# Performance work log

Hardware: AMD Instinct MI355X
Metric: run time of the kernel (lower is better)

The kernel has to match this reference:

```python
import jax, jax.numpy as jnp
import numpy as np

B, S, D_IN, D_OUT = 8, 2048, 1024, 1024

def setup_inputs() -> dict:
    key = jax.random.key(0)
    ks = jax.random.split(key, 6)
    return {
        "inputs_for_keys": jax.random.normal(ks[0], (B, S, D_IN), dtype=jnp.float32),
        "inputs_for_values": jax.random.normal(ks[1], (B, S, D_IN), dtype=jnp.float32),
        "inputs_for_queries": jax.random.normal(ks[2], (B, S, D_IN), dtype=jnp.float32),
        "W_K": jax.random.normal(ks[3], (D_IN, D_OUT), dtype=jnp.float32) * 0.05,
        "W_V": jax.random.normal(ks[4], (D_IN, D_OUT), dtype=jnp.float32) * 0.05,
        "W_Q": jax.random.normal(ks[5], (D_IN, D_OUT), dtype=jnp.float32) * 0.05,
    }

def reference(inputs_for_keys, inputs_for_values, inputs_for_queries, W_K, W_V, W_Q):
    # Linear projections: [B,S,D_in] @ [D_in,D_out] -> [B,S,D_out]
    K = jnp.einsum("bsd,de->bse", inputs_for_keys, W_K)
    V = jnp.einsum("bsd,de->bse", inputs_for_values, W_V)
    Q = jnp.einsum("bsd,de->bse", inputs_for_queries, W_Q)
    scale = jnp.sqrt(jnp.asarray(K.shape[-1], dtype=K.dtype))
    # Scaled dot-product attention scores: [B,Sq,Sk]
    scores = jnp.einsum("bqe,bke->bqk", Q, K) / scale
    probs = jax.nn.softmax(scores, axis=-1)
    Z = jnp.einsum("bqk,bke->bqe", probs, V)
    return Z
```

## Files before the change

### kernel.cpp

```cpp
#include <hip/hip_runtime.h>
#include <hip/hip_bf16.h>
#include <stdint.h>

#define BATCH 8
#define SEQ 2048
#define DMODEL 1024

typedef __attribute__((ext_vector_type(4))) float f32x4;
typedef __attribute__((ext_vector_type(8))) short bf16x8;
typedef __attribute__((ext_vector_type(4))) uint32_t u32x4;
typedef __attribute__((ext_vector_type(2))) uint32_t u32x2;

#define MFMA16(a, b, c) __builtin_amdgcn_mfma_f32_16x16x32_bf16((a), (b), (c), 0, 0, 0)


static __device__ __forceinline__ uint16_t f2bf(float f) {
    uint32_t u = __builtin_bit_cast(uint32_t, f);
    u += 0x7fffu + ((u >> 16) & 1u);
    return (uint16_t)(u >> 16);
}
static __device__ __forceinline__ uint32_t pk2(float lo, float hi) {
    return (uint32_t)f2bf(lo) | ((uint32_t)f2bf(hi) << 16);
}
static __device__ __forceinline__ void gload16(const uint16_t* g, uint16_t* l) {
    __builtin_amdgcn_global_load_lds((const __attribute__((address_space(1))) void*)g,
                                     (__attribute__((address_space(3))) void*)l, 16, 0, 0);
}

__global__ __launch_bounds__(256) void cast_bf16_pk(const float* __restrict__ src,
                                                    uint16_t* __restrict__ dst) {
    const size_t c = (size_t)blockIdx.x * 256 + threadIdx.x;
    const size_t panel = c >> 11;
    const int w = (int)(c & 2047);
    const int ks = w >> 4, r15 = w & 15;
    const float* s = src + (panel * 16 + r15) * DMODEL + ks * 8;
    f32x4 a = *(const f32x4*)s;
    f32x4 b = *(const f32x4*)(s + 4);
    u32x4 o = {pk2(a[0], a[1]), pk2(a[2], a[3]), pk2(b[0], b[1]), pk2(b[2], b[3])};
    *(u32x4*)(dst + c * 8) = o;
}

__global__ void wt_cast_kernel(const float* __restrict__ Wk, const float* __restrict__ Wv,
                               const float* __restrict__ Wq, uint16_t* __restrict__ WT) {
    const float* W = blockIdx.z == 0 ? Wk : (blockIdx.z == 1 ? Wv : Wq);
    uint16_t* dst = WT + (size_t)blockIdx.z * DMODEL * DMODEL;
    __shared__ float tile[32][33];
    const int x = blockIdx.x * 32, y = blockIdx.y * 32;
    const int tx = threadIdx.x, ty = threadIdx.y;
#pragma unroll
    for (int j = 0; j < 4; j++)
        tile[ty * 4 + j][tx] = W[(size_t)(y + ty * 4 + j) * DMODEL + x + tx];
    __syncthreads();
#pragma unroll
    for (int j = 0; j < 4; j++) {
        const int n = x + ty * 4 + j, k = y + tx;
        const size_t off = ((size_t)(n >> 4) * (DMODEL / 8) + (k >> 3)) * 128 +
                           (n & 15) * 8 + (k & 7);
        dst[off] = f2bf(tile[tx][ty * 4 + j]);
    }
}

#define STG_A(kt, sl, h)                                                          \
    do {                                                                          \
        const size_t g0 = (size_t)((h) * 8 + (tid >> 7)) * eldA +                 \
                          (size_t)(kt) * 1024 + (tid & 127) * 8;                  \
        gload16(Ab + g0, &As[sl][(h) * 8192 + tid * 8]);                          \
        gload16(Ab + g0 + 4 * eldA, &As[sl][(h) * 8192 + tid * 8 + 4096]);        \
    } while (0)
#define STG_B(kt, sl, h)                                                          \
    do {                                                                          \
        const size_t g0 = (size_t)((h) * 8 + (tid >> 7)) * eldB +                 \
                          (size_t)(kt) * 1024 + (tid & 127) * 8;                  \
        gload16(Bb + g0, &Bs[sl][(h) * 8192 + tid * 8]);                          \
        gload16(Bb + g0 + 4 * eldB, &Bs[sl][(h) * 8192 + tid * 8 + 4096]);        \
    } while (0)

#define READ_B(sl)                                                                \
    _Pragma("unroll") for (int j = 0; j < 4; j++) {                               \
        bfr[j][0] = *(const bf16x8*)&Bs[sl][(wc * 4 + j) * 1024 + lbase];         \
        bfr[j][1] = *(const bf16x8*)&Bs[sl][(wc * 4 + j) * 1024 + 512 + lbase];   \
    }

#define VM4 asm volatile("s_waitcnt vmcnt(4)" ::: "memory")
#define VM0 asm volatile("s_waitcnt vmcnt(0)" ::: "memory")
#define NOPW (void)0
#define NOST (void)0

#define PH(sl, q, STG, WAIT)                                                      \
    do {                                                                          \
        const int ab = (wr * 8 + 2 * (q)) * 1024 + lbase;                         \
        bf16x8 a00 = *(const bf16x8*)&As[sl][ab];                                 \
        bf16x8 a01 = *(const bf16x8*)&As[sl][ab + 512];                           \
        bf16x8 a10 = *(const bf16x8*)&As[sl][ab + 1024];                          \
        bf16x8 a11 = *(const bf16x8*)&As[sl][ab + 1536];                          \
        STG;                                                                      \
        WAIT;                                                                     \
        __builtin_amdgcn_s_barrier();                                             \
        asm volatile("s_waitcnt lgkmcnt(0)" ::: "memory");                        \
        __builtin_amdgcn_sched_barrier(0);                                        \
        __builtin_amdgcn_s_setprio(1);                                            \
        _Pragma("unroll") for (int j = 0; j < 4; j++) {                           \
            acc[2 * (q)][j] = MFMA16(a00, bfr[j][0], acc[2 * (q)][j]);            \
            acc[2 * (q)][j] = MFMA16(a01, bfr[j][1], acc[2 * (q)][j]);            \
            acc[2 * (q) + 1][j] = MFMA16(a10, bfr[j][0], acc[2 * (q) + 1][j]);    \
            acc[2 * (q) + 1][j] = MFMA16(a11, bfr[j][1], acc[2 * (q) + 1][j]);    \
        }                                                                         \
        __builtin_amdgcn_s_setprio(0);                                            \
        __builtin_amdgcn_s_barrier();                                             \
    } while (0)

template <int MODE, int BX>
__global__ __launch_bounds__(512, 2) void gemm8p(const uint16_t* __restrict__ Ag,
                                                 const uint16_t* __restrict__ Bg,
                                                 void* __restrict__ Cg,
                                                 const float* __restrict__ Linv,
                                                 float scale, int lda, int ldb, int ldc,
                                                 int nk, size_t sA, size_t sB, size_t sC) {
    __shared__ __align__(16) uint16_t As[2][16384];
    __shared__ __align__(16) uint16_t Bs[2][16384];
    const int bz = BX ? blockIdx.x : blockIdx.z;
    const int bm = BX ? blockIdx.y : blockIdx.x;
    const int bn = BX ? blockIdx.z : blockIdx.y;
    const int m0 = bm * 256, n0 = bn * 256;
    const uint16_t* Ab = Ag + (size_t)bz * sA + (size_t)m0 * lda;
    const uint16_t* Bb = Bg + (size_t)bz * sB + (size_t)n0 * ldb;
    const int tid = threadIdx.x, lane = tid & 63;
    const int wid = tid >> 6, wr = wid >> 2, wc = wid & 3;
    const int lr = lane & 15, lg = lane >> 4;
    const int lbase = lg * 128 + lr * 8;
    const size_t eldA = (size_t)lda * 16, eldB = (size_t)ldb * 16;

    f32x4 acc[8][4] = {};
    bf16x8 bfr[4][2];
    STG_A(0, 0, 0); STG_A(0, 0, 1);
    STG_B(0, 0, 0); STG_B(0, 0, 1);
    STG_B(1, 1, 0); STG_B(1, 1, 1);
    VM4;
    __builtin_amdgcn_s_barrier();
    for (int kt = 0; kt + 3 < nk; kt += 2) {
        READ_B(0);
        PH(0, 0, STG_A(kt + 1, 1, 0), NOPW);
        PH(0, 1, STG_A(kt + 1, 1, 1), NOPW);
        PH(0, 2, STG_B(kt + 2, 0, 0), NOPW);
        PH(0, 3, STG_B(kt + 2, 0, 1), VM4);
        READ_B(1);
        PH(1, 0, STG_A(kt + 2, 0, 0), NOPW);
        PH(1, 1, STG_A(kt + 2, 0, 1), NOPW);
        PH(1, 2, STG_B(kt + 3, 1, 0), NOPW);
        PH(1, 3, STG_B(kt + 3, 1, 1), VM4);
    }
    READ_B(0);
    PH(0, 0, STG_A(nk - 1, 1, 0), NOPW);
    PH(0, 1, STG_A(nk - 1, 1, 1), NOPW);
    PH(0, 2, NOST, NOPW);
    PH(0, 3, NOST, VM0);
    READ_B(1);
    PH(1, 0, NOST, NOPW);
    PH(1, 1, NOST, NOPW);
    PH(1, 2, NOST, NOPW);
    PH(1, 3, NOST, NOPW);

    if constexpr (MODE == 0) {
        uint16_t* C = (uint16_t*)Cg + (size_t)bz * sC;
#pragma unroll
        for (int i = 0; i < 8; i++) {
            const int gm = m0 + wr * 128 + i * 16 + lg * 4;
            const size_t pbase = (size_t)(gm >> 4) * (ldc / 8);
#pragma unroll
            for (int j = 0; j < 4; j++) {
                const int gn = n0 + wc * 64 + j * 16 + lr;
                const size_t off = (pbase + (gn >> 3)) * 128 + (gn & 7);
#pragma unroll
                for (int r = 0; r < 4; r++)
                    C[off + (lg * 4 + r) * 8] = f2bf(acc[i][j][r] * scale);
            }
        }
    } else if constexpr (MODE == 1) {
        uint16_t* C = (uint16_t*)Cg;
#pragma unroll
        for (int i = 0; i < 8; i++) {
            const int gm = m0 + wr * 128 + i * 16 + lg * 4;
            const int bb = gm / SEQ;
            const int s0 = gm - bb * SEQ;
            uint16_t* Cb = C + (size_t)bb * DMODEL * SEQ;
#pragma unroll
            for (int j = 0; j < 4; j++) {
                const int e = n0 + wc * 64 + j * 16 + lr;
                const size_t off = ((size_t)(e >> 4) * (SEQ / 8) + (s0 >> 3)) * 128 +
                                   (e & 15) * 8 + (s0 & 7);
                u32x2 v = {pk2(acc[i][j][0], acc[i][j][1]), pk2(acc[i][j][2], acc[i][j][3])};
                *(u32x2*)&Cb[off] = v;
            }
        }
    } else {
        float* C = (float*)Cg + (size_t)bz * sC;
        const float* LB = Linv + bz * SEQ;
#pragma unroll
        for (int i = 0; i < 8; i++) {
            const int gm = m0 + wr * 128 + i * 16 + lg * 4;
            const f32x4 lv = *(const f32x4*)&LB[gm];
#pragma unroll
            for (int j = 0; j < 4; j++) {
                const int gn = n0 + wc * 64 + j * 16 + lr;
#pragma unroll
                for (int r = 0; r < 4; r++)
                    C[(size_t)(gm + r) * ldc + gn] = acc[i][j][r] * lv[r];
            }
        }
    }
}

__global__ __launch_bounds__(256) void softmax_pk(uint16_t* __restrict__ S,
                                                  float* __restrict__ Linv) {
    const size_t panel = blockIdx.x;
    uint16_t* sp = S + panel * (size_t)(16 * SEQ);
    const int t = threadIdx.x, lane = t & 63, w = t >> 6;
    const int r15 = t & 15, ksl = t >> 4;
    __shared__ float rm[4][16], rs[4][16];
    u32x4 raw[16];
    float mx = -3.0e38f;
#pragma unroll
    for (int u = 0; u < 16; u++) {
        raw[u] = *(const u32x4*)&sp[(ksl + u * 16) * 128 + r15 * 8];
#pragma unroll
        for (int j = 0; j < 4; j++) {
            mx = fmaxf(mx, __builtin_bit_cast(float, raw[u][j] << 16));
            mx = fmaxf(mx, __builtin_bit_cast(float, raw[u][j] & 0xffff0000u));
        }
    }
    mx = fmaxf(mx, __shfl_xor(mx, 16));
    mx = fmaxf(mx, __shfl_xor(mx, 32));
    if (lane < 16) rm[w][lane] = mx;
    __syncthreads();
    const float m = fmaxf(fmaxf(rm[0][r15], rm[1][r15]), fmaxf(rm[2][r15], rm[3][r15]));
    float sum = 0.0f;
#pragma unroll
    for (int u = 0; u < 16; u++) {
#pragma unroll
        for (int j = 0; j < 4; j++) {
            float lo = __expf(__builtin_bit_cast(float, raw[u][j] << 16) - m);
            float hi = __expf(__builtin_bit_cast(float, raw[u][j] & 0xffff0000u) - m);
            sum += lo + hi;
            raw[u][j] = pk2(lo, hi);
        }
    }
    sum += __shfl_xor(sum, 16);
    sum += __shfl_xor(sum, 32);
    if (lane < 16) rs[w][lane] = sum;
    __syncthreads();
    const float tot = rs[0][r15] + rs[1][r15] + rs[2][r15] + rs[3][r15];
#pragma unroll
    for (int u = 0; u < 16; u++)
        *(u32x4*)&sp[(ksl + u * 16) * 128 + r15 * 8] = raw[u];
    if (w == 0 && lane < 16) Linv[panel * 16 + lane] = 1.0f / tot;
}

extern "C" void kernel_launch(void* const* d_in, const int* in_sizes, int n_in,
                              void* d_out, int out_size, void* d_ws, size_t ws_size,
                              hipStream_t stream) {
    const float* Xk = (const float*)d_in[0];
    const float* Xv = (const float*)d_in[1];
    const float* Xq = (const float*)d_in[2];
    const float* Wk = (const float*)d_in[3];
    const float* Wv = (const float*)d_in[4];
    const float* Wq = (const float*)d_in[5];
    float* out = (float*)d_out;
    char* ws = (char*)d_ws;
    uint16_t* Qbf = (uint16_t*)(ws);
    uint16_t* Kbf = (uint16_t*)(ws + (size_t)33554432);
    uint16_t* VTb = (uint16_t*)(ws + (size_t)67108864);
    uint16_t* WT  = (uint16_t*)(ws + (size_t)100663296);
    float*    Linv= (float*)(ws + (size_t)106954752);
    uint16_t* Sb  = (uint16_t*)(ws + (size_t)107020288);
    uint16_t* Xbf = (uint16_t*)(ws + (size_t)171966464);

    wt_cast_kernel<<<dim3(32, 32, 3), dim3(32, 8), 0, stream>>>(Wk, Wv, Wq, WT);
    cast_bf16_pk<<<8192, 256, 0, stream>>>(Xq, Xbf);
    gemm8p<0, 0><<<dim3(64, 4, 1), 512, 0, stream>>>(
        Xbf, WT + 2 * 1048576, (void*)Qbf, nullptr, 0.03125f,
        DMODEL, DMODEL, DMODEL, DMODEL / 64, 0, 0, 0);
    cast_bf16_pk<<<8192, 256, 0, stream>>>(Xk, Xbf);
    gemm8p<0, 0><<<dim3(64, 4, 1), 512, 0, stream>>>(
        Xbf, WT, (void*)Kbf, nullptr, 1.0f,
        DMODEL, DMODEL, DMODEL, DMODEL / 64, 0, 0, 0);
    cast_bf16_pk<<<8192, 256, 0, stream>>>(Xv, Xbf);
    gemm8p<1, 0><<<dim3(64, 4, 1), 512, 0, stream>>>(
        Xbf, WT + 1048576, (void*)VTb, nullptr, 1.0f,
        DMODEL, DMODEL, 0, DMODEL / 64, 0, 0, 0);
    gemm8p<0, 1><<<dim3(8, 8, 8), 512, 0, stream>>>(
        Qbf, Kbf, (void*)Sb, nullptr, 1.0f,
        DMODEL, DMODEL, SEQ, DMODEL / 64,
        (size_t)SEQ * DMODEL, (size_t)SEQ * DMODEL, (size_t)SEQ * SEQ);
    softmax_pk<<<dim3(BATCH * SEQ / 16), 256, 0, stream>>>(Sb, Linv);
    gemm8p<2, 1><<<dim3(8, 8, 4), 512, 0, stream>>>(
        Sb, VTb, (void*)out, Linv, 1.0f,
        SEQ, SEQ, DMODEL, SEQ / 64,
        (size_t)SEQ * SEQ, (size_t)DMODEL * SEQ, (size_t)SEQ * DMODEL);
}
```

Baseline: 369.7 us.

## Shrink GEMM tiles to 128x128 with 4-wave blocks for more parallelism

Replaces the 256x256-tile, 8-wave GEMM with a 128x128-tile, 4-wave variant that keeps the same double-buffered, phase-interleaved load/MFMA pipeline. The stage loads and per-phase fragments are rearranged for the smaller tiles, and all GEMM launches get four times as many blocks. The aim is better CU occupancy and load balance, since the old grids (256 or 512 blocks) poorly filled the GPU. The cost is lower data reuse per block, so more global and L2 traffic per FLOP, plus more barriers relative to compute.

```diff
diff --git a/kernel.cpp b/kernel.cpp
--- a/kernel.cpp
+++ b/kernel.cpp
@@ -60,111 +60,120 @@
     }
 }
 
-#define STG_A(kt, sl, h)                                                          \
-    do {                                                                          \
-        const size_t g0 = (size_t)((h) * 8 + (tid >> 7)) * eldA +                 \
-                          (size_t)(kt) * 1024 + (tid & 127) * 8;                  \
-        gload16(Ab + g0, &As[sl][(h) * 8192 + tid * 8]);                          \
-        gload16(Ab + g0 + 4 * eldA, &As[sl][(h) * 8192 + tid * 8 + 4096]);        \
+#define STG_A(kt, sl)                                                         \
+    do {                                                                      \
+        const size_t k0_ = (size_t)(kt) * 1024;                               \
+        gload16(Ab + k0_ + sbA,            &As[sl][tid * 8]);                 \
+        gload16(Ab + k0_ + sbA + 2 * eldA, &As[sl][tid * 8 + 2048]);          \
+        gload16(Ab + k0_ + sbA + 4 * eldA, &As[sl][tid * 8 + 4096]);          \
+        gload16(Ab + k0_ + sbA + 6 * eldA, &As[sl][tid * 8 + 6144]);          \
     } while (0)
-#define STG_B(kt, sl, h)                                                          \
-    do {                                                                          \
-        const size_t g0 = (size_t)((h) * 8 + (tid >> 7)) * eldB +                 \
-                          (size_t)(kt) * 1024 + (tid & 127) * 8;                  \
-        gload16(Bb + g0, &Bs[sl][(h) * 8192 + tid * 8]);                          \
-        gload16(Bb + g0 + 4 * eldB, &Bs[sl][(h) * 8192 + tid * 8 + 4096]);        \
+#define STG_B(kt, sl)                                                         \
+    do {                                                                      \
+        const size_t k0_ = (size_t)(kt) * 1024;                               \
+        gload16(Bb + k0_ + sbB,            &Bs[sl][tid * 8]);                 \
+        gload16(Bb + k0_ + sbB + 2 * eldB, &Bs[sl][tid * 8 + 2048]);          \
+        gload16(Bb + k0_ + sbB + 4 * eldB, &Bs[sl][tid * 8 + 4096]);          \
+        gload16(Bb + k0_ + sbB + 6 * eldB, &Bs[sl][tid * 8 + 6144]);          \
     } while (0)
 
-#define READ_B(sl)                                                                \
-    _Pragma("unroll") for (int j = 0; j < 4; j++) {                               \
-        bfr[j][0] = *(const bf16x8*)&Bs[sl][(wc * 4 + j) * 1024 + lbase];         \
-        bfr[j][1] = *(const bf16x8*)&Bs[sl][(wc * 4 + j) * 1024 + 512 + lbase];   \
-    }
-
-#define VM4 asm volatile("s_waitcnt vmcnt(4)" ::: "memory")
-#define VM0 asm volatile("s_waitcnt vmcnt(0)" ::: "memory")
-#define NOPW (void)0
+#define READ_B(sl)                                                            \
+    _Pragma("unroll") for (int j = 0; j < 4; j++) {                           \
+        bfr[j][0] = *(const bf16x8*)&Bs[sl][(wc * 4 + j) * 1024 + lbase];     \
+        bfr[j][1] = *(const bf16x8*)&Bs[sl][(wc * 4 + j) * 1024 + 512 + lbase]; \
+    }
+
+#define VMW4 asm volatile("s_waitcnt vmcnt(4)" ::: "memory")
+#define VMW0 asm volatile("s_waitcnt vmcnt(0)" ::: "memory")
+#define NOW (void)0
 #define NOST (void)0
 
-#define PH(sl, q, STG, WAIT)                                                      \
-    do {                                                                          \
-        const int ab = (wr * 8 + 2 * (q)) * 1024 + lbase;                         \
-        bf16x8 a00 = *(const bf16x8*)&As[sl][ab];                                 \
-        bf16x8 a01 = *(const bf16x8*)&As[sl][ab + 512];                           \
-        bf16x8 a10 = *(const bf16x8*)&As[sl][ab + 1024];                          \
-        bf16x8 a11 = *(const bf16x8*)&As[sl][ab + 1536];                          \
-        STG;                                                                      \
-        WAIT;                                                                     \
-        __builtin_amdgcn_s_barrier();                                             \
-        asm volatile("s_waitcnt lgkmcnt(0)" ::: "memory");                        \
-        __builtin_amdgcn_sched_barrier(0);                                        \
-        __builtin_amdgcn_s_setprio(1);                                            \
-        _Pragma("unroll") for (int j = 0; j < 4; j++) {                           \
-            acc[2 * (q)][j] = MFMA16(a00, bfr[j][0], acc[2 * (q)][j]);            \
-            acc[2 * (q)][j] = MFMA16(a01, bfr[j][1], acc[2 * (q)][j]);            \
-            acc[2 * (q) + 1][j] = MFMA16(a10, bfr[j][0], acc[2 * (q) + 1][j]);    \
-            acc[2 * (q) + 1][j] = MFMA16(a11, bfr[j][1], acc[2 * (q) + 1][j]);    \
-        }                                                                         \
-        __builtin_amdgcn_s_setprio(0);                                            \
-        __builtin_amdgcn_s_barrier();                                             \
+#define PH_CORE(r0, r1)                                                       \
+    __builtin_amdgcn_s_barrier();                                             \
+    asm volatile("s_waitcnt lgkmcnt(0)" ::: "memory");                        \
+    __builtin_amdgcn_sched_barrier(0);                                        \
+    __builtin_amdgcn_s_setprio(1);                                            \
+    _Pragma("unroll") for (int j = 0; j < 4; j++) {                           \
+        acc[r0][j] = MFMA16(a00, bfr[j][0], acc[r0][j]);                      \
+        acc[r0][j] = MFMA16(a01, bfr[j][1], acc[r0][j]);                      \
+        acc[r1][j] = MFMA16(a10, bfr[j][0], acc[r1][j]);                      \
+        acc[r1][j] = MFMA16(a11, bfr[j][1], acc[r1][j]);                      \
+    }                                                                         \
+    __builtin_amdgcn_s_setprio(0);                                            \
+    __builtin_amdgcn_s_barrier();
+
+#define PH0(sl, STG, WAIT)                                                    \
+    do {                                                                      \
+        READ_B(sl);                                                           \
+        const int ab_ = (wr * 4) * 1024 + lbase;                              \
+        bf16x8 a00 = *(const bf16x8*)&As[sl][ab_];                            \
+        bf16x8 a01 = *(const bf16x8*)&As[sl][ab_ + 512];                      \
+        bf16x8 a10 = *(const bf16x8*)&As[sl][ab_ + 1024];                     \
+        bf16x8 a11 = *(const bf16x8*)&As[sl][ab_ + 1536];                     \
+        STG;                                                                  \
+        WAIT;                                                                 \
+        PH_CORE(0, 1)                                                         \
     } while (0)
 
+#define PH1(sl, STG, WAIT)                                                    \
+    do {                                                                      \
+        const int ab_ = (wr * 4 + 2) * 1024 + lbase;                          \
+        bf16x8 a00 = *(const bf16x8*)&As[sl][ab_];                            \
+        bf16x8 a01 = *(const bf16x8*)&As[sl][ab_ + 512];                      \
+        bf16x8 a10 = *(const bf16x8*)&As[sl][ab_ + 1024];                     \
+        bf16x8 a11 = *(const bf16x8*)&As[sl][ab_ + 1536];                     \
+        STG;                                                                  \
+        WAIT;                                                                 \
+        PH_CORE(2, 3)                                                         \
+    } while (0)
+
 template <int MODE, int BX>
-__global__ __launch_bounds__(512, 2) void gemm8p(const uint16_t* __restrict__ Ag,
-                                                 const uint16_t* __restrict__ Bg,
-                                                 void* __restrict__ Cg,
-                                                 const float* __restrict__ Linv,
-                                                 float scale, int lda, int ldb, int ldc,
-                                                 int nk, size_t sA, size_t sB, size_t sC) {
-    __shared__ __align__(16) uint16_t As[2][16384];
-    __shared__ __align__(16) uint16_t Bs[2][16384];
+__global__ __launch_bounds__(256, 2) void gemm128(const uint16_t* __restrict__ Ag,
+                                                  const uint16_t* __restrict__ Bg,
+                                                  void* __restrict__ Cg,
+                                                  const float* __restrict__ Linv,
+                                                  float scale, int lda, int ldb, int ldc,
+                                                  int nk, size_t sA, size_t sB, size_t sC) {
+    __shared__ __align__(16) uint16_t As[2][8192];
+    __shared__ __align__(16) uint16_t Bs[2][8192];
     const int bz = BX ? blockIdx.x : blockIdx.z;
     const int bm = BX ? blockIdx.y : blockIdx.x;
     const int bn = BX ? blockIdx.z : blockIdx.y;
-    const int m0 = bm * 256, n0 = bn * 256;
+    const int m0 = bm * 128, n0 = bn * 128;
     const uint16_t* Ab = Ag + (size_t)bz * sA + (size_t)m0 * lda;
     const uint16_t* Bb = Bg + (size_t)bz * sB + (size_t)n0 * ldb;
     const int tid = threadIdx.x, lane = tid & 63;
-    const int wid = tid >> 6, wr = wid >> 2, wc = wid & 3;
+    const int wid = tid >> 6, wr = wid >> 1, wc = wid & 1;
     const int lr = lane & 15, lg = lane >> 4;
     const int lbase = lg * 128 + lr * 8;
     const size_t eldA = (size_t)lda * 16, eldB = (size_t)ldb * 16;
-
-    f32x4 acc[8][4] = {};
+    const size_t sbA = (size_t)(tid >> 7) * eldA + (tid & 127) * 8;
+    const size_t sbB = (size_t)(tid >> 7) * eldB + (tid & 127) * 8;
+
+    f32x4 acc[4][4] = {};
     bf16x8 bfr[4][2];
-    STG_A(0, 0, 0); STG_A(0, 0, 1);
-    STG_B(0, 0, 0); STG_B(0, 0, 1);
-    STG_B(1, 1, 0); STG_B(1, 1, 1);
-    VM4;
+    STG_B(0, 0);
+    STG_A(0, 0);
+    STG_B(1, 1);
+    VMW4;
     __builtin_amdgcn_s_barrier();
-    for (int kt = 0; kt + 3 < nk; kt += 2) {
-        READ_B(0);
-        PH(0, 0, STG_A(kt + 1, 1, 0), NOPW);
-        PH(0, 1, STG_A(kt + 1, 1, 1), NOPW);
-        PH(0, 2, STG_B(kt + 2, 0, 0), NOPW);
-        PH(0, 3, STG_B(kt + 2, 0, 1), VM4);
-        READ_B(1);
-        PH(1, 0, STG_A(kt + 2, 0, 0), NOPW);
-        PH(1, 1, STG_A(kt + 2, 0, 1), NOPW);
-        PH(1, 2, STG_B(kt + 3, 1, 0), NOPW);
-        PH(1, 3, STG_B(kt + 3, 1, 1), VM4);
-    }
-    READ_B(0);
-    PH(0, 0, STG_A(nk - 1, 1, 0), NOPW);
-    PH(0, 1, STG_A(nk - 1, 1, 1), NOPW);
-    PH(0, 2, NOST, NOPW);
-    PH(0, 3, NOST, VM0);
-    READ_B(1);
-    PH(1, 0, NOST, NOPW);
-    PH(1, 1, NOST, NOPW);
-    PH(1, 2, NOST, NOPW);
-    PH(1, 3, NOST, NOPW);
+    for (int J = 0; J < nk / 2 - 1; ++J) {
+        const int t2 = 2 * J;
+        PH0(0, STG_A(t2 + 1, 1), NOW);
+        PH1(0, STG_B(t2 + 2, 0), VMW4);
+        PH0(1, STG_A(t2 + 2, 0), NOW);
+        PH1(1, STG_B(t2 + 3, 1), VMW4);
+    }
+    PH0(0, STG_A(nk - 1, 1), NOW);
+    PH1(0, NOST, VMW0);
+    PH0(1, NOST, NOW);
+    PH1(1, NOST, NOW);
 
     if constexpr (MODE == 0) {
         uint16_t* C = (uint16_t*)Cg + (size_t)bz * sC;
 #pragma unroll
-        for (int i = 0; i < 8; i++) {
-            const int gm = m0 + wr * 128 + i * 16 + lg * 4;
+        for (int i = 0; i < 4; i++) {
+            const int gm = m0 + wr * 64 + i * 16 + lg * 4;
             const size_t pbase = (size_t)(gm >> 4) * (ldc / 8);
 #pragma unroll
             for (int j = 0; j < 4; j++) {
@@ -178,8 +187,8 @@
     } else if constexpr (MODE == 1) {
         uint16_t* C = (uint16_t*)Cg;
 #pragma unroll
-        for (int i = 0; i < 8; i++) {
-            const int gm = m0 + wr * 128 + i * 16 + lg * 4;
+        for (int i = 0; i < 4; i++) {
+            const int gm = m0 + wr * 64 + i * 16 + lg * 4;
             const int bb = gm / SEQ;
             const int s0 = gm - bb * SEQ;
             uint16_t* Cb = C + (size_t)bb * DMODEL * SEQ;
@@ -196,8 +205,8 @@
         float* C = (float*)Cg + (size_t)bz * sC;
         const float* LB = Linv + bz * SEQ;
 #pragma unroll
-        for (int i = 0; i < 8; i++) {
-            const int gm = m0 + wr * 128 + i * 16 + lg * 4;
+        for (int i = 0; i < 4; i++) {
+            const int gm = m0 + wr * 64 + i * 16 + lg * 4;
             const f32x4 lv = *(const f32x4*)&LB[gm];
 #pragma unroll
             for (int j = 0; j < 4; j++) {
@@ -276,23 +285,23 @@
 
     wt_cast_kernel<<<dim3(32, 32, 3), dim3(32, 8), 0, stream>>>(Wk, Wv, Wq, WT);
     cast_bf16_pk<<<8192, 256, 0, stream>>>(Xq, Xbf);
-    gemm8p<0, 0><<<dim3(64, 4, 1), 512, 0, stream>>>(
+    gemm128<0, 0><<<dim3(128, 8, 1), 256, 0, stream>>>(
         Xbf, WT + 2 * 1048576, (void*)Qbf, nullptr, 0.03125f,
         DMODEL, DMODEL, DMODEL, DMODEL / 64, 0, 0, 0);
     cast_bf16_pk<<<8192, 256, 0, stream>>>(Xk, Xbf);
-    gemm8p<0, 0><<<dim3(64, 4, 1), 512, 0, stream>>>(
+    gemm128<0, 0><<<dim3(128, 8, 1), 256, 0, stream>>>(
         Xbf, WT, (void*)Kbf, nullptr, 1.0f,
         DMODEL, DMODEL, DMODEL, DMODEL / 64, 0, 0, 0);
     cast_bf16_pk<<<8192, 256, 0, stream>>>(Xv, Xbf);
-    gemm8p<1, 0><<<dim3(64, 4, 1), 512, 0, stream>>>(
+    gemm128<1, 0><<<dim3(128, 8, 1), 256, 0, stream>>>(
         Xbf, WT + 1048576, (void*)VTb, nullptr, 1.0f,
         DMODEL, DMODEL, 0, DMODEL / 64, 0, 0, 0);
-    gemm8p<0, 1><<<dim3(8, 8, 8), 512, 0, stream>>>(
+    gemm128<0, 1><<<dim3(8, 16, 16), 256, 0, stream>>>(
         Qbf, Kbf, (void*)Sb, nullptr, 1.0f,
         DMODEL, DMODEL, SEQ, DMODEL / 64,
         (size_t)SEQ * DMODEL, (size_t)SEQ * DMODEL, (size_t)SEQ * SEQ);
     softmax_pk<<<dim3(BATCH * SEQ / 16), 256, 0, stream>>>(Sb, Linv);
-    gemm8p<2, 1><<<dim3(8, 8, 4), 512, 0, stream>>>(
+    gemm128<2, 1><<<dim3(8, 16, 8), 256, 0, stream>>>(
         Sb, VTb, (void*)out, Linv, 1.0f,
         SEQ, SEQ, DMODEL, SEQ / 64,
         (size_t)SEQ * SEQ, (size_t)DMODEL * SEQ, (size_t)SEQ * DMODEL);
```

Result: slower. 384.1 us (+3.9%).

## Batch Q/K/V casts and projections into single launches, trim per-phase barriers

Applied to the files above, without the earlier changes.

Merges the three fp32-to-bf16 input casts into one launch and the three projection GEMMs into one batched launch (MODE 3). The batched launch picks its A operand, weight slice and output layout from blockIdx.z, giving 768 blocks instead of three sequential 256-block launches, so the GPU should fill better and launch overhead drops. The cast buffers are placed in the output buffer and the scores buffer, which are free at that point, so the three bf16 copies need no extra workspace. It also removes the trailing barrier from all but the last phase of each k-step, cutting synchronisation, at some risk of LDS reuse hazards if a later phase's staging overlaps data still being read.

```diff
diff --git a/kernel.cpp b/kernel.cpp
--- a/kernel.cpp
+++ b/kernel.cpp
@@ -27,8 +27,15 @@
                                      (__attribute__((address_space(3))) void*)l, 16, 0, 0);
 }
 
-__global__ __launch_bounds__(256) void cast_bf16_pk(const float* __restrict__ src,
-                                                    uint16_t* __restrict__ dst) {
+__global__ __launch_bounds__(256) void cast3_bf16_pk(const float* __restrict__ x0,
+                                                     const float* __restrict__ x1,
+                                                     const float* __restrict__ x2,
+                                                     uint16_t* __restrict__ d0,
+                                                     uint16_t* __restrict__ d1,
+                                                     uint16_t* __restrict__ d2) {
+    const int z = blockIdx.y;
+    const float* src = z == 0 ? x0 : (z == 1 ? x1 : x2);
+    uint16_t* dst = z == 0 ? d0 : (z == 1 ? d1 : d2);
     const size_t c = (size_t)blockIdx.x * 256 + threadIdx.x;
     const size_t panel = c >> 11;
     const int w = (int)(c & 2047);
@@ -85,8 +92,10 @@
 #define VM0 asm volatile("s_waitcnt vmcnt(0)" ::: "memory")
 #define NOPW (void)0
 #define NOST (void)0
-
-#define PH(sl, q, STG, WAIT)                                                      \
+#define ENDBAR __builtin_amdgcn_s_barrier()
+#define NOB (void)0
+
+#define PH(sl, q, STG, WAIT, EB)                                                  \
     do {                                                                          \
         const int ab = (wr * 8 + 2 * (q)) * 1024 + lbase;                         \
         bf16x8 a00 = *(const bf16x8*)&As[sl][ab];                                 \
@@ -106,7 +115,7 @@
             acc[2 * (q) + 1][j] = MFMA16(a11, bfr[j][1], acc[2 * (q) + 1][j]);    \
         }                                                                         \
         __builtin_amdgcn_s_setprio(0);                                            \
-        __builtin_amdgcn_s_barrier();                                             \
+        EB;                                                                       \
     } while (0)
 
 template <int MODE, int BX>
@@ -115,15 +124,27 @@
                                                  void* __restrict__ Cg,
                                                  const float* __restrict__ Linv,
                                                  float scale, int lda, int ldb, int ldc,
-                                                 int nk, size_t sA, size_t sB, size_t sC) {
+                                                 int nk, size_t sA, size_t sB, size_t sC,
+                                                 const uint16_t* __restrict__ A2,
+                                                 const uint16_t* __restrict__ A3,
+                                                 void* __restrict__ C2,
+                                                 void* __restrict__ C3) {
     __shared__ __align__(16) uint16_t As[2][16384];
     __shared__ __align__(16) uint16_t Bs[2][16384];
     const int bz = BX ? blockIdx.x : blockIdx.z;
     const int bm = BX ? blockIdx.y : blockIdx.x;
     const int bn = BX ? blockIdx.z : blockIdx.y;
     const int m0 = bm * 256, n0 = bn * 256;
-    const uint16_t* Ab = Ag + (size_t)bz * sA + (size_t)m0 * lda;
-    const uint16_t* Bb = Bg + (size_t)bz * sB + (size_t)n0 * ldb;
+    const uint16_t *Abase, *Bbase;
+    if constexpr (MODE == 3) {
+        Abase = (bz == 0) ? Ag : (bz == 1) ? A2 : A3;
+        Bbase = Bg + ((bz == 0) ? 2 * sB : (bz == 1) ? (size_t)0 : sB);
+    } else {
+        Abase = Ag + (size_t)bz * sA;
+        Bbase = Bg + (size_t)bz * sB;
+    }
+    const uint16_t* Ab = Abase + (size_t)m0 * lda;
+    const uint16_t* Bb = Bbase + (size_t)n0 * ldb;
     const int tid = threadIdx.x, lane = tid & 63;
     const int wid = tid >> 6, wr = wid >> 2, wc = wid & 3;
     const int lr = lane & 15, lg = lane >> 4;
@@ -139,26 +160,26 @@
     __builtin_amdgcn_s_barrier();
     for (int kt = 0; kt + 3 < nk; kt += 2) {
         READ_B(0);
-        PH(0, 0, STG_A(kt + 1, 1, 0), NOPW);
-        PH(0, 1, STG_A(kt + 1, 1, 1), NOPW);
-        PH(0, 2, STG_B(kt + 2, 0, 0), NOPW);
-        PH(0, 3, STG_B(kt + 2, 0, 1), VM4);
+        PH(0, 0, STG_A(kt + 1, 1, 0), NOPW, NOB);
+        PH(0, 1, STG_A(kt + 1, 1, 1), NOPW, NOB);
+        PH(0, 2, STG_B(kt + 2, 0, 0), NOPW, NOB);
+        PH(0, 3, STG_B(kt + 2, 0, 1), VM4, ENDBAR);
         READ_B(1);
-        PH(1, 0, STG_A(kt + 2, 0, 0), NOPW);
-        PH(1, 1, STG_A(kt + 2, 0, 1), NOPW);
-        PH(1, 2, STG_B(kt + 3, 1, 0), NOPW);
-        PH(1, 3, STG_B(kt + 3, 1, 1), VM4);
+        PH(1, 0, STG_A(kt + 2, 0, 0), NOPW, NOB);
+        PH(1, 1, STG_A(kt + 2, 0, 1), NOPW, NOB);
+        PH(1, 2, STG_B(kt + 3, 1, 0), NOPW, NOB);
+        PH(1, 3, STG_B(kt + 3, 1, 1), VM4, ENDBAR);
     }
     READ_B(0);
-    PH(0, 0, STG_A(nk - 1, 1, 0), NOPW);
-    PH(0, 1, STG_A(nk - 1, 1, 1), NOPW);
-    PH(0, 2, NOST, NOPW);
-    PH(0, 3, NOST, VM0);
+    PH(0, 0, STG_A(nk - 1, 1, 0), NOPW, NOB);
+    PH(0, 1, STG_A(nk - 1, 1, 1), NOPW, NOB);
+    PH(0, 2, NOST, NOPW, NOB);
+    PH(0, 3, NOST, VM0, ENDBAR);
     READ_B(1);
-    PH(1, 0, NOST, NOPW);
-    PH(1, 1, NOST, NOPW);
-    PH(1, 2, NOST, NOPW);
-    PH(1, 3, NOST, NOPW);
+    PH(1, 0, NOST, NOPW, NOB);
+    PH(1, 1, NOST, NOPW, NOB);
+    PH(1, 2, NOST, NOPW, NOB);
+    PH(1, 3, NOST, NOPW, NOB);
 
     if constexpr (MODE == 0) {
         uint16_t* C = (uint16_t*)Cg + (size_t)bz * sC;
@@ -192,7 +213,7 @@
                 *(u32x2*)&Cb[off] = v;
             }
         }
-    } else {
+    } else if constexpr (MODE == 2) {
         float* C = (float*)Cg + (size_t)bz * sC;
         const float* LB = Linv + bz * SEQ;
 #pragma unroll
@@ -205,6 +226,42 @@
 #pragma unroll
                 for (int r = 0; r < 4; r++)
                     C[(size_t)(gm + r) * ldc + gn] = acc[i][j][r] * lv[r];
+            }
+        }
+    } else {
+        if (bz < 2) {
+            uint16_t* C = (uint16_t*)(bz == 0 ? Cg : C2);
+            const float sc = bz == 0 ? scale : 1.0f;
+#pragma unroll
+            for (int i = 0; i < 8; i++) {
+                const int gm = m0 + wr * 128 + i * 16 + lg * 4;
+                const size_t pbase = (size_t)(gm >> 4) * (ldc / 8);
+#pragma unroll
+                for (int j = 0; j < 4; j++) {
+                    const int gn = n0 + wc * 64 + j * 16 + lr;
+                    const size_t off = (pbase + (gn >> 3)) * 128 + (gn & 7);
+#pragma unroll
+                    for (int r = 0; r < 4; r++)
+                        C[off + (lg * 4 + r) * 8] = f2bf(acc[i][j][r] * sc);
+                }
+            }
+        } else {
+            uint16_t* C = (uint16_t*)C3;
+#pragma unroll
+            for (int i = 0; i < 8; i++) {
+                const int gm = m0 + wr * 128 + i * 16 + lg * 4;
+                const int bb = gm / SEQ;
+                const int s0 = gm - bb * SEQ;
+                uint16_t* Cb = C + (size_t)bb * DMODEL * SEQ;
+#pragma unroll
+                for (int j = 0; j < 4; j++) {
+                    const int e = n0 + wc * 64 + j * 16 + lr;
+                    const size_t off = ((size_t)(e >> 4) * (SEQ / 8) + (s0 >> 3)) * 128 +
+                                       (e & 15) * 8 + (s0 & 7);
+                    u32x2 v = {pk2(acc[i][j][0], acc[i][j][1]),
+                               pk2(acc[i][j][2], acc[i][j][3])};
+                    *(u32x2*)&Cb[off] = v;
+                }
             }
         }
     }
@@ -272,28 +329,26 @@
     uint16_t* WT  = (uint16_t*)(ws + (size_t)100663296);
     float*    Linv= (float*)(ws + (size_t)106954752);
     uint16_t* Sb  = (uint16_t*)(ws + (size_t)107020288);
-    uint16_t* Xbf = (uint16_t*)(ws + (size_t)171966464);
+    uint16_t* XqB = (uint16_t*)d_out;
+    uint16_t* XkB = Sb;
+    uint16_t* XvB = (uint16_t*)(ws + (size_t)140574720);
 
     wt_cast_kernel<<<dim3(32, 32, 3), dim3(32, 8), 0, stream>>>(Wk, Wv, Wq, WT);
-    cast_bf16_pk<<<8192, 256, 0, stream>>>(Xq, Xbf);
-    gemm8p<0, 0><<<dim3(64, 4, 1), 512, 0, stream>>>(
-        Xbf, WT + 2 * 1048576, (void*)Qbf, nullptr, 0.03125f,
-        DMODEL, DMODEL, DMODEL, DMODEL / 64, 0, 0, 0);
-    cast_bf16_pk<<<8192, 256, 0, stream>>>(Xk, Xbf);
-    gemm8p<0, 0><<<dim3(64, 4, 1), 512, 0, stream>>>(
-        Xbf, WT, (void*)Kbf, nullptr, 1.0f,
-        DMODEL, DMODEL, DMODEL, DMODEL / 64, 0, 0, 0);
-    cast_bf16_pk<<<8192, 256, 0, stream>>>(Xv, Xbf);
-    gemm8p<1, 0><<<dim3(64, 4, 1), 512, 0, stream>>>(
-        Xbf, WT + 1048576, (void*)VTb, nullptr, 1.0f,
-        DMODEL, DMODEL, 0, DMODEL / 64, 0, 0, 0);
+    cast3_bf16_pk<<<dim3(8192, 3), 256, 0, stream>>>(Xq, Xk, Xv, XqB, XkB, XvB);
+    gemm8p<3, 0><<<dim3(64, 4, 3), 512, 0, stream>>>(
+        XqB, WT, (void*)Qbf, nullptr, 0.03125f,
+        DMODEL, DMODEL, DMODEL, DMODEL / 64,
+        0, (size_t)1048576 , 0,
+        XkB, XvB, (void*)Kbf, (void*)VTb);
     gemm8p<0, 1><<<dim3(8, 8, 8), 512, 0, stream>>>(
         Qbf, Kbf, (void*)Sb, nullptr, 1.0f,
         DMODEL, DMODEL, SEQ, DMODEL / 64,
-        (size_t)SEQ * DMODEL, (size_t)SEQ * DMODEL, (size_t)SEQ * SEQ);
+        (size_t)SEQ * DMODEL, (size_t)SEQ * DMODEL, (size_t)SEQ * SEQ,
+        nullptr, nullptr, nullptr, nullptr);
     softmax_pk<<<dim3(BATCH * SEQ / 16), 256, 0, stream>>>(Sb, Linv);
     gemm8p<2, 1><<<dim3(8, 8, 4), 512, 0, stream>>>(
         Sb, VTb, (void*)out, Linv, 1.0f,
         SEQ, SEQ, DMODEL, SEQ / 64,
-        (size_t)SEQ * SEQ, (size_t)DMODEL * SEQ, (size_t)SEQ * DMODEL);
-}
+        (size_t)SEQ * SEQ, (size_t)DMODEL * SEQ, (size_t)SEQ * DMODEL,
+        nullptr, nullptr, nullptr, nullptr);
+}
```

After: 343.1 us. 1.08x faster.
